# Kernel optimization log

Hardware: AMD Instinct MI355X
Metric: run time of the kernel (lower is better)

Reference implementation:

```python
import jax, jax.numpy as jnp
import numpy as np

B, S, HID = 4, 2048, 1024
H, DH = 16, 64  # HID = H * DH
ADP, NTASKS = 64, 10
GATE_S = 100.0  # s (soft gate temperature), != smax=400 so no hard threshold


def setup_inputs() -> dict:
    key = jax.random.key(0)
    ks = jax.random.split(key, 13)
    sc = 0.02
    return {
        "hidden_states": jax.random.normal(ks[0], (B, S, HID), jnp.float32),
        "Wq": jax.random.normal(ks[1], (HID, HID), jnp.float32) * sc,
        "bq": jax.random.normal(ks[2], (HID,), jnp.float32) * sc,
        "Wk": jax.random.normal(ks[3], (HID, HID), jnp.float32) * sc,
        "bk": jax.random.normal(ks[4], (HID,), jnp.float32) * sc,
        "Wv": jax.random.normal(ks[5], (HID, HID), jnp.float32) * sc,
        "bv": jax.random.normal(ks[6], (HID,), jnp.float32) * sc,
        "fc1_w": jax.random.normal(ks[7], (HID, ADP), jnp.float32) * sc,
        "fc1_b": jax.random.normal(ks[8], (ADP,), jnp.float32) * sc,
        "fc2_w": jax.random.normal(ks[9], (ADP, HID), jnp.float32) * sc,
        "fc2_b": jax.random.normal(ks[10], (HID,), jnp.float32) * sc,
        "efc1": jax.random.normal(ks[11], (NTASKS, ADP), jnp.float32),
        "efc2": jax.random.normal(ks[12], (NTASKS, HID), jnp.float32),
        "t": 3,
    }


def reference(hidden_states, Wq, bq, Wk, bk, Wv, bv,
              fc1_w, fc1_b, fc2_w, fc2_b, efc1, efc2, t):
    x = hidden_states
    # --- parallel adapter with task gates (add_residual=False) ---
    gfc1 = jax.nn.sigmoid(GATE_S * efc1[t])  # [ADP]
    gfc2 = jax.nn.sigmoid(GATE_S * efc2[t])  # [HID]
    h = jax.nn.relu(x @ fc1_w + fc1_b) * gfc1          # [B,S,ADP]
    adapter_out = jax.nn.relu(h @ fc2_w + fc2_b) * gfc2  # [B,S,HID]
    # --- multi-head self-attention (absolute positions, no mask, eval dropout) ---
    def split_heads(y):  # [B,S,HID] -> [B,H,S,DH]
        return y.reshape(B, S, H, DH).transpose(0, 2, 1, 3)
    q = split_heads(x @ Wq + bq)
    k = split_heads(x @ Wk + bk)
    v = split_heads(x @ Wv + bv)
    scores = jnp.einsum("bhqd,bhkd->bhqk", q, k) / np.sqrt(DH).astype(jnp.float32)
    probs = jax.nn.softmax(scores, axis=-1)
    ctx = jnp.einsum("bhqk,bhkd->bhqd", probs, v)
    ctx = ctx.transpose(0, 2, 1, 3).reshape(B, S, HID)
    return ctx + adapter_out
```

## Files before the change

kernel.cpp:

```cpp
#include <hip/hip_runtime.h>
#include <stdint.h>
#include <stddef.h>

typedef unsigned short u16;
typedef unsigned int u32;
typedef __bf16 bf16x8 __attribute__((ext_vector_type(8)));
typedef __bf16 bf16x4 __attribute__((ext_vector_type(4)));
typedef short s16x4 __attribute__((ext_vector_type(4)));
typedef float f32x4 __attribute__((ext_vector_type(4)));

#define BB  4
#define SS  2048
#define HIDD 1024
#define NH  16
#define DHD 64

#define GLD16(gaddr, laddr) \
  __builtin_amdgcn_global_load_lds( \
      (const __attribute__((address_space(1))) u32*)(gaddr), \
      (__attribute__((address_space(3))) u32*)(laddr), 16, 0, 0)

#define LDS_BARRIER() asm volatile("s_waitcnt lgkmcnt(0)\n\ts_barrier" ::: "memory")

#if __has_builtin(__builtin_amdgcn_exp2f)
  #define EXP2(x) __builtin_amdgcn_exp2f(x)
#else
  #define EXP2(x) __expf((x) * 0.6931471805599453f)
#endif

__device__ __forceinline__ u16 f2b(float f){
  union { float f; unsigned u; } c; c.f = f;
  unsigned r = c.u + 0x7fffu + ((c.u >> 16) & 1u);
  return (u16)(r >> 16);
}
__device__ __forceinline__ f32x4 mfma32(bf16x8 a, bf16x8 b, f32x4 c){
  return __builtin_amdgcn_mfma_f32_16x16x32_bf16(a, b, c, 0, 0, 0);
}
__device__ __forceinline__ f32x4 mfma16(s16x4 a, s16x4 b, f32x4 c){
  return __builtin_amdgcn_mfma_f32_16x16x16bf16_1k(a, b, c, 0, 0, 0);
}

__global__ __launch_bounds__(256)
void prep(const float* __restrict__ x, u16* __restrict__ xb,
          const float* __restrict__ Wq, const float* __restrict__ Wk,
          const float* __restrict__ Wv, const float* __restrict__ f1w,
          const float* __restrict__ f2w,
          u16* __restrict__ wqkv, u16* __restrict__ wtf1, u16* __restrict__ wtf2)
{
  __shared__ float tile[32][33];
  int blk = blockIdx.x;
  const int tid = threadIdx.x;
  if (blk < 8192) {
    int i = blk * 1024 + tid * 4;
    float4 v = *reinterpret_cast<const float4*>(&x[i]);
    ushort4 o;
    o.x = f2b(v.x); o.y = f2b(v.y); o.z = f2b(v.z); o.w = f2b(v.w);
    *reinterpret_cast<ushort4*>(&xb[i]) = o;
    return;
  }
  blk -= 8192;
  if (blk >= 3200) {
    u16* pad = wqkv + (size_t)3136 * 1024;
    uint4 z = make_uint4(0u, 0u, 0u, 0u);
    *reinterpret_cast<uint4*>(&pad[(size_t)(blk - 3200) * 2048 + tid * 8]) = z;
    return;
  }
  const float* in; u16* out; int R, C, c0, r0;
  if (blk < 3072) {
    int m = blk >> 10, t = blk & 1023;
    in = (m == 0) ? Wq : (m == 1) ? Wk : Wv;
    out = wqkv + (size_t)m * 1024 * 1024;
    R = 1024; C = 1024; c0 = (t & 31) * 32; r0 = (t >> 5) * 32;
  } else if (blk < 3136) {
    int t = blk - 3072;
    in = f1w; out = wtf1; R = 1024; C = 64;
    c0 = (t & 1) * 32; r0 = (t >> 1) * 32;
  } else {
    int t = blk - 3136;
    in = f2w; out = wtf2; R = 64; C = 1024;
    c0 = (t & 31) * 32; r0 = (t >> 5) * 32;
  }
  int tx = tid & 31, ty = tid >> 5;
  #pragma unroll
  for (int j = 0; j < 32; j += 8)
    tile[ty + j][tx] = in[(size_t)(r0 + ty + j) * C + c0 + tx];
  __syncthreads();
  #pragma unroll
  for (int j = 0; j < 32; j += 8)
    out[(size_t)(c0 + ty + j) * R + r0 + tx] = f2b(tile[tx][ty + j]);
}

__global__ __launch_bounds__(256)
void gemm_qkv(const u16* __restrict__ X, const u16* __restrict__ Wt,
              const float* __restrict__ bq, const float* __restrict__ bk,
              const float* __restrict__ bv,
              const float* __restrict__ f1b, const float* __restrict__ efc1,
              const int* __restrict__ tptr,
              u16* __restrict__ qb, u16* __restrict__ kb, u16* __restrict__ vt,
              u16* __restrict__ hb)
{
  constexpr int K = 1024;
  __shared__ __align__(16) u16 ldsX[128 * 32];
  __shared__ __align__(16) u16 ldsW[128 * 32];
  const int tid = threadIdx.x;
  const int w = tid >> 6, lane = tid & 63, quad = lane >> 4, ln = lane & 15;
  const int m0 = blockIdx.y * 128, n0 = blockIdx.x * 128;
  const int wrow = (w >> 1) * 64;
  const int wcol = (w & 1) * 64;
  const int srow = tid >> 2;
  const int scol = (tid & 3) * 8;

  f32x4 acc[4][4] = {};

  for (int k0 = 0; k0 < K; k0 += 32) {
    #pragma unroll
    for (int c = 0; c < 2; ++c)
      GLD16(&X[(size_t)(m0 + c * 64 + srow) * K + k0 + scol], &ldsX[c * 2048 + w * 512]);
    #pragma unroll
    for (int c = 0; c < 2; ++c)
      GLD16(&Wt[(size_t)(n0 + c * 64 + srow) * K + k0 + scol], &ldsW[c * 2048 + w * 512]);
    __syncthreads();

    bf16x8 a[4], bfr[4];
    #pragma unroll
    for (int mt = 0; mt < 4; ++mt)
      a[mt] = *reinterpret_cast<const bf16x8*>(&ldsX[(wrow + mt * 16 + ln) * 32 + quad * 8]);
    #pragma unroll
    for (int nt = 0; nt < 4; ++nt)
      bfr[nt] = *reinterpret_cast<const bf16x8*>(&ldsW[(wcol + nt * 16 + ln) * 32 + quad * 8]);
    #pragma unroll
    for (int mt = 0; mt < 4; ++mt)
      #pragma unroll
      for (int nt = 0; nt < 4; ++nt)
        acc[mt][nt] = mfma32(a[mt], bfr[nt], acc[mt][nt]);
    __syncthreads();
  }

  if (n0 < 2048) {
    const float scale = (n0 < 1024) ? 0.18033688f : 1.f;
    const float* bias = (n0 < 1024) ? bq : bk;
    u16* dst = (n0 < 1024) ? qb : kb;
    const int nb = n0 & 1023;
    #pragma unroll
    for (int nt = 0; nt < 4; ++nt) {
      const int col = nb + wcol + nt * 16 + ln;
      const float bvv = bias[col];
      #pragma unroll
      for (int mt = 0; mt < 4; ++mt)
        #pragma unroll
        for (int r = 0; r < 4; ++r) {
          int row = m0 + wrow + mt * 16 + quad * 4 + r;
          dst[(size_t)row * 1024 + col] = f2b((acc[mt][nt][r] + bvv) * scale);
        }
    }
  } else if (n0 < 3072) {
    #pragma unroll
    for (int nt = 0; nt < 4; ++nt) {
      const int colv = (n0 - 2048) + wcol + nt * 16 + ln;
      const float bvv = bv[colv];
      const int h = colv >> 6, d = colv & 63;
      #pragma unroll
      for (int mt = 0; mt < 4; ++mt) {
        int row = m0 + wrow + mt * 16 + quad * 4;
        int bb = row >> 11, s = row & 2047;
        ushort4 o;
        o.x = f2b(acc[mt][nt][0] + bvv);
        o.y = f2b(acc[mt][nt][1] + bvv);
        o.z = f2b(acc[mt][nt][2] + bvv);
        o.w = f2b(acc[mt][nt][3] + bvv);
        *reinterpret_cast<ushort4*>(
            &vt[((((size_t)bb * NH + h) * DHD + d) << 11) + s]) = o;
      }
    }
  } else if (wcol == 0) {
    int t = tptr[0];
    if ((unsigned)t > 9u) t = 0;
    #pragma unroll
    for (int nt = 0; nt < 4; ++nt) {
      const int col = nt * 16 + ln;
      const float bvv = f1b[col];
      const float g = 1.f / (1.f + __expf(-100.f * efc1[t * 64 + col]));
      #pragma unroll
      for (int mt = 0; mt < 4; ++mt)
        #pragma unroll
        for (int r = 0; r < 4; ++r) {
          int row = m0 + wrow + mt * 16 + quad * 4 + r;
          hb[(size_t)row * 64 + col] = f2b(fmaxf(acc[mt][nt][r] + bvv, 0.f) * g);
        }
    }
  }
}

__global__ __launch_bounds__(256, 4)
void attn(const u16* __restrict__ Q, const u16* __restrict__ Kb,
          const u16* __restrict__ Vt, const u16* __restrict__ hb,
          const u16* __restrict__ w2, const float* __restrict__ b2,
          const float* __restrict__ gate2, const int* __restrict__ tptr,
          float* __restrict__ out)
{
  __shared__ __align__(16) u16 ldsK[64 * 72];
  __shared__ __align__(16) u16 ldsV[64 * 76];

  const int tid = threadIdx.x;
  const int w = tid >> 6, lane = tid & 63, quad = lane >> 4, ln = lane & 15;
  const int h = blockIdx.x, b = blockIdx.y, qt = blockIdx.z;
  const int bh = b * NH + h;
  const int qbase = qt * 128 + w * 32;
  const int skey = tid >> 3;
  const int sd   = (tid & 7) * 8;

  bf16x8 qf[2][2];
  #pragma unroll
  for (int q2 = 0; q2 < 2; ++q2)
    #pragma unroll
    for (int kk = 0; kk < 2; ++kk)
      qf[q2][kk] = *reinterpret_cast<const bf16x8*>(
          &Q[(size_t)(b * SS + qbase + q2 * 16 + ln) * HIDD + h * DHD + kk * 32 + quad * 8]);

  f32x4 o[4][2] = {};
  f32x4 lacc[2] = {};
  const s16x4 ones = {0x3F80, 0x3F80, 0x3F80, 0x3F80};

  const u16* Kp = &Kb[(size_t)(b * SS + skey) * HIDD + h * DHD + sd];
  const u16* Vp = &Vt[((size_t)bh * DHD + skey) * SS + sd];

  uint4 rK0 = *reinterpret_cast<const uint4*>(Kp);
  uint4 rK1 = *reinterpret_cast<const uint4*>(Kp + (size_t)32 * HIDD);
  uint4 rV0 = *reinterpret_cast<const uint4*>(Vp);
  uint4 rV1 = *reinterpret_cast<const uint4*>(Vp + (size_t)32 * SS);

  for (int kt = 0; kt < SS; kt += 64) {
    LDS_BARRIER();
    *reinterpret_cast<uint4*>(&ldsK[skey * 72 + sd])        = rK0;
    *reinterpret_cast<uint4*>(&ldsK[(32 + skey) * 72 + sd]) = rK1;
    *reinterpret_cast<uint4*>(&ldsV[skey * 76 + sd])        = rV0;
    *reinterpret_cast<uint4*>(&ldsV[(32 + skey) * 76 + sd]) = rV1;
    if (kt + 64 < SS) {
      const u16* Kn = Kp + (size_t)(kt + 64) * HIDD;
      const u16* Vn = Vp + (kt + 64);
      rK0 = *reinterpret_cast<const uint4*>(Kn);
      rK1 = *reinterpret_cast<const uint4*>(Kn + (size_t)32 * HIDD);
      rV0 = *reinterpret_cast<const uint4*>(Vn);
      rV1 = *reinterpret_cast<const uint4*>(Vn + (size_t)32 * SS);
    }
    LDS_BARRIER();

    f32x4 s[4][2];
    __builtin_amdgcn_s_setprio(1);
    #pragma unroll
    for (int k4 = 0; k4 < 4; ++k4) {
      bf16x8 kf0 = *reinterpret_cast<const bf16x8*>(&ldsK[(k4 * 16 + ln) * 72 + quad * 8]);
      bf16x8 kf1 = *reinterpret_cast<const bf16x8*>(&ldsK[(k4 * 16 + ln) * 72 + 32 + quad * 8]);
      #pragma unroll
      for (int q2 = 0; q2 < 2; ++q2) {
        f32x4 z = {0.f, 0.f, 0.f, 0.f};
        z = mfma32(kf0, qf[q2][0], z);
        z = mfma32(kf1, qf[q2][1], z);
        s[k4][q2] = z;
      }
    }
    __builtin_amdgcn_s_setprio(0);

    s16x4 p[4][2];
    #pragma unroll
    for (int k4 = 0; k4 < 4; ++k4)
      #pragma unroll
      for (int q2 = 0; q2 < 2; ++q2) {
        union { bf16x4 b; s16x4 s; } cv;
        #pragma unroll
        for (int r = 0; r < 4; ++r)
          cv.b[r] = (__bf16)EXP2(s[k4][q2][r]);
        p[k4][q2] = cv.s;
      }

    __builtin_amdgcn_s_setprio(1);
    #pragma unroll
    for (int dt = 0; dt < 4; ++dt) {
      #pragma unroll
      for (int ks = 0; ks < 4; ++ks) {
        s16x4 vf = *reinterpret_cast<const s16x4*>(
            &ldsV[(dt * 16 + ln) * 76 + ks * 16 + quad * 4]);
        #pragma unroll
        for (int q2 = 0; q2 < 2; ++q2)
          o[dt][q2] = mfma16(vf, p[ks][q2], o[dt][q2]);
      }
    }
    #pragma unroll
    for (int ks = 0; ks < 4; ++ks)
      #pragma unroll
      for (int q2 = 0; q2 < 2; ++q2)
        lacc[q2] = mfma16(ones, p[ks][q2], lacc[q2]);
    __builtin_amdgcn_s_setprio(0);
  }

  float rl[2];
  #pragma unroll
  for (int q2 = 0; q2 < 2; ++q2)
    rl[q2] = 1.f / lacc[q2][0];

  f32x4 acc2[4][2] = {};
  #pragma unroll
  for (int kk = 0; kk < 2; ++kk) {
    bf16x8 hf[2];
    #pragma unroll
    for (int q2 = 0; q2 < 2; ++q2) {
      int q = qbase + q2 * 16 + ln;
      hf[q2] = *reinterpret_cast<const bf16x8*>(
          &hb[(size_t)(b * SS + q) * 64 + kk * 32 + quad * 8]);
    }
    #pragma unroll
    for (int dt = 0; dt < 4; ++dt) {
      bf16x8 wf = *reinterpret_cast<const bf16x8*>(
          &w2[(size_t)(h * DHD + dt * 16 + ln) * 64 + kk * 32 + quad * 8]);
      #pragma unroll
      for (int q2 = 0; q2 < 2; ++q2)
        acc2[dt][q2] = mfma32(wf, hf[q2], acc2[dt][q2]);
    }
  }

  int t = tptr[0];
  if ((unsigned)t > 9u) t = 0;
  float bv2[4][4], gv2[4][4];
  #pragma unroll
  for (int dt = 0; dt < 4; ++dt)
    #pragma unroll
    for (int r = 0; r < 4; ++r) {
      int col = h * DHD + dt * 16 + quad * 4 + r;
      bv2[dt][r] = b2[col];
      gv2[dt][r] = 1.f / (1.f + __expf(-100.f * gate2[t * HIDD + col]));
    }

  #pragma unroll
  for (int q2 = 0; q2 < 2; ++q2) {
    const int q = qbase + q2 * 16 + ln;
    float* orow = &out[(size_t)(b * SS + q) * HIDD + h * DHD];
    #pragma unroll
    for (int dt = 0; dt < 4; ++dt)
      #pragma unroll
      for (int r = 0; r < 4; ++r) {
        int d = dt * 16 + quad * 4 + r;
        float ad = fmaxf(acc2[dt][q2][r] + bv2[dt][r], 0.f) * gv2[dt][r];
        orow[d] = o[dt][q2][r] * rl[q2] + ad;
      }
  }
}

extern "C" void kernel_launch(void* const* d_in, const int* in_sizes, int n_in,
                              void* d_out, int out_size, void* d_ws, size_t ws_size,
                              hipStream_t stream) {
  const float* x    = (const float*)d_in[0];
  const float* Wq   = (const float*)d_in[1];
  const float* bq   = (const float*)d_in[2];
  const float* Wk   = (const float*)d_in[3];
  const float* bk   = (const float*)d_in[4];
  const float* Wv   = (const float*)d_in[5];
  const float* bv   = (const float*)d_in[6];
  const float* f1w  = (const float*)d_in[7];
  const float* f1b  = (const float*)d_in[8];
  const float* f2w  = (const float*)d_in[9];
  const float* f2b_ = (const float*)d_in[10];
  const float* efc1 = (const float*)d_in[11];
  const float* efc2 = (const float*)d_in[12];
  const int*   tptr = (const int*)d_in[13];
  float* out = (float*)d_out;

  unsigned char* ws = (unsigned char*)d_ws;
  u16* xb   = (u16*)(ws + 0);
  u16* wqkv = (u16*)(ws + (16u << 20));
  u16* wtf1 = wqkv + (size_t)3072 * 1024;
  u16* wtf2 = (u16*)(ws + (22u << 20) + (256u << 10));
  u16* hb   = (u16*)(ws + (23u << 20));
  u16* qb   = (u16*)(ws + (24u << 20));
  u16* kb   = (u16*)(ws + (40u << 20));
  u16* vt   = (u16*)(ws + (56u << 20));

  prep<<<dim3(11424), 256, 0, stream>>>(x, xb, Wq, Wk, Wv, f1w, f2w,
                                        wqkv, wtf1, wtf2);

  gemm_qkv<<<dim3(25, 64), 256, 0, stream>>>(xb, wqkv, bq, bk, bv,
                                             f1b, efc1, tptr, qb, kb, vt, hb);

  attn<<<dim3(NH, BB, SS / 128), 256, 0, stream>>>(
      qb, kb, vt, hb, wtf2, f2b_, efc2, tptr, out);
}
```

Measured before the change: 292.1 us.

## Double-buffer QKV GEMM, swizzle blocks, and compute softmax sums on VALU

The QKV GEMM now double-buffers its LDS tiles so the global-to-LDS loads for the next K slice are issued before computing the current one. It also uses a 1D grid with a swizzled block-to-tile mapping to improve L2 reuse. In attention, the row sums come from per-lane VALU accumulation of the fp32 exponentials plus a cross-lane shuffle, replacing extra MFMAs against a ones vector. The exp-to-bf16 conversion uses a cheaper rounding, and the s_setprio hints are removed. Doubled LDS may reduce GEMM occupancy, and the denominator now uses unrounded fp32 values while the numerator uses bf16-rounded ones.

```diff
diff --git a/kernel.cpp b/kernel.cpp
--- a/kernel.cpp
+++ b/kernel.cpp
@@ -5,7 +5,6 @@
 typedef unsigned short u16;
 typedef unsigned int u32;
 typedef __bf16 bf16x8 __attribute__((ext_vector_type(8)));
-typedef __bf16 bf16x4 __attribute__((ext_vector_type(4)));
 typedef short s16x4 __attribute__((ext_vector_type(4)));
 typedef float f32x4 __attribute__((ext_vector_type(4)));
 
@@ -32,6 +31,10 @@
   union { float f; unsigned u; } c; c.f = f;
   unsigned r = c.u + 0x7fffu + ((c.u >> 16) & 1u);
   return (u16)(r >> 16);
+}
+__device__ __forceinline__ u16 f2b_fast(float f){
+  union { float f; unsigned u; } c; c.f = f;
+  return (u16)((c.u + 0x8000u) >> 16);
 }
 __device__ __forceinline__ f32x4 mfma32(bf16x8 a, bf16x8 b, f32x4 c){
   return __builtin_amdgcn_mfma_f32_16x16x32_bf16(a, b, c, 0, 0, 0);
@@ -100,11 +103,14 @@
               u16* __restrict__ hb)
 {
   constexpr int K = 1024;
-  __shared__ __align__(16) u16 ldsX[128 * 32];
-  __shared__ __align__(16) u16 ldsW[128 * 32];
+  __shared__ __align__(16) u16 ldsX[2][128 * 32];
+  __shared__ __align__(16) u16 ldsW[2][128 * 32];
   const int tid = threadIdx.x;
   const int w = tid >> 6, lane = tid & 63, quad = lane >> 4, ln = lane & 15;
-  const int m0 = blockIdx.y * 128, n0 = blockIdx.x * 128;
+  const int id = blockIdx.x;
+  const int swz = (id & 7) * 200 + (id >> 3);
+  const int m0 = (swz / 25) * 128;
+  const int n0 = (swz % 25) * 128;
   const int wrow = (w >> 1) * 64;
   const int wcol = (w & 1) * 64;
   const int srow = tid >> 2;
@@ -112,27 +118,40 @@
 
   f32x4 acc[4][4] = {};
 
-  for (int k0 = 0; k0 < K; k0 += 32) {
-    #pragma unroll
-    for (int c = 0; c < 2; ++c)
-      GLD16(&X[(size_t)(m0 + c * 64 + srow) * K + k0 + scol], &ldsX[c * 2048 + w * 512]);
-    #pragma unroll
-    for (int c = 0; c < 2; ++c)
-      GLD16(&Wt[(size_t)(n0 + c * 64 + srow) * K + k0 + scol], &ldsW[c * 2048 + w * 512]);
-    __syncthreads();
+  #pragma unroll
+  for (int c = 0; c < 2; ++c) {
+    GLD16(&X[(size_t)(m0 + c * 64 + srow) * K + scol], &ldsX[0][c * 2048 + w * 512]);
+    GLD16(&Wt[(size_t)(n0 + c * 64 + srow) * K + scol], &ldsW[0][c * 2048 + w * 512]);
+  }
+  __syncthreads();
+
+  int cur = 0;
+  for (int k0 = 0; k0 < K; k0 += 32, cur ^= 1) {
+    if (k0 + 32 < K) {
+      #pragma unroll
+      for (int c = 0; c < 2; ++c) {
+        GLD16(&X[(size_t)(m0 + c * 64 + srow) * K + k0 + 32 + scol],
+              &ldsX[cur ^ 1][c * 2048 + w * 512]);
+        GLD16(&Wt[(size_t)(n0 + c * 64 + srow) * K + k0 + 32 + scol],
+              &ldsW[cur ^ 1][c * 2048 + w * 512]);
+      }
+    }
 
     bf16x8 a[4], bfr[4];
     #pragma unroll
     for (int mt = 0; mt < 4; ++mt)
-      a[mt] = *reinterpret_cast<const bf16x8*>(&ldsX[(wrow + mt * 16 + ln) * 32 + quad * 8]);
+      a[mt] = *reinterpret_cast<const bf16x8*>(
+          &ldsX[cur][(wrow + mt * 16 + ln) * 32 + quad * 8]);
     #pragma unroll
     for (int nt = 0; nt < 4; ++nt)
-      bfr[nt] = *reinterpret_cast<const bf16x8*>(&ldsW[(wcol + nt * 16 + ln) * 32 + quad * 8]);
+      bfr[nt] = *reinterpret_cast<const bf16x8*>(
+          &ldsW[cur][(wcol + nt * 16 + ln) * 32 + quad * 8]);
     #pragma unroll
     for (int mt = 0; mt < 4; ++mt)
       #pragma unroll
       for (int nt = 0; nt < 4; ++nt)
         acc[mt][nt] = mfma32(a[mt], bfr[nt], acc[mt][nt]);
+
     __syncthreads();
   }
 
@@ -218,8 +237,7 @@
           &Q[(size_t)(b * SS + qbase + q2 * 16 + ln) * HIDD + h * DHD + kk * 32 + quad * 8]);
 
   f32x4 o[4][2] = {};
-  f32x4 lacc[2] = {};
-  const s16x4 ones = {0x3F80, 0x3F80, 0x3F80, 0x3F80};
+  float lsum[2] = {0.f, 0.f};
 
   const u16* Kp = &Kb[(size_t)(b * SS + skey) * HIDD + h * DHD + sd];
   const u16* Vp = &Vt[((size_t)bh * DHD + skey) * SS + sd];
@@ -246,7 +264,6 @@
     LDS_BARRIER();
 
     f32x4 s[4][2];
-    __builtin_amdgcn_s_setprio(1);
     #pragma unroll
     for (int k4 = 0; k4 < 4; ++k4) {
       bf16x8 kf0 = *reinterpret_cast<const bf16x8*>(&ldsK[(k4 * 16 + ln) * 72 + quad * 8]);
@@ -259,21 +276,19 @@
         s[k4][q2] = z;
       }
     }
-    __builtin_amdgcn_s_setprio(0);
 
     s16x4 p[4][2];
     #pragma unroll
     for (int k4 = 0; k4 < 4; ++k4)
       #pragma unroll
-      for (int q2 = 0; q2 < 2; ++q2) {
-        union { bf16x4 b; s16x4 s; } cv;
+      for (int q2 = 0; q2 < 2; ++q2)
         #pragma unroll
-        for (int r = 0; r < 4; ++r)
-          cv.b[r] = (__bf16)EXP2(s[k4][q2][r]);
-        p[k4][q2] = cv.s;
-      }
-
-    __builtin_amdgcn_s_setprio(1);
+        for (int r = 0; r < 4; ++r) {
+          float pv = EXP2(s[k4][q2][r]);
+          lsum[q2] += pv;
+          p[k4][q2][r] = (short)f2b_fast(pv);
+        }
+
     #pragma unroll
     for (int dt = 0; dt < 4; ++dt) {
       #pragma unroll
@@ -285,18 +300,16 @@
           o[dt][q2] = mfma16(vf, p[ks][q2], o[dt][q2]);
       }
     }
-    #pragma unroll
-    for (int ks = 0; ks < 4; ++ks)
-      #pragma unroll
-      for (int q2 = 0; q2 < 2; ++q2)
-        lacc[q2] = mfma16(ones, p[ks][q2], lacc[q2]);
-    __builtin_amdgcn_s_setprio(0);
   }
 
   float rl[2];
   #pragma unroll
-  for (int q2 = 0; q2 < 2; ++q2)
-    rl[q2] = 1.f / lacc[q2][0];
+  for (int q2 = 0; q2 < 2; ++q2) {
+    float v = lsum[q2];
+    v += __shfl_xor(v, 16);
+    v += __shfl_xor(v, 32);
+    rl[q2] = 1.f / v;
+  }
 
   f32x4 acc2[4][2] = {};
   #pragma unroll
@@ -377,8 +390,8 @@
   prep<<<dim3(11424), 256, 0, stream>>>(x, xb, Wq, Wk, Wv, f1w, f2w,
                                         wqkv, wtf1, wtf2);
 
-  gemm_qkv<<<dim3(25, 64), 256, 0, stream>>>(xb, wqkv, bq, bk, bv,
-                                             f1b, efc1, tptr, qb, kb, vt, hb);
+  gemm_qkv<<<dim3(1600), 256, 0, stream>>>(xb, wqkv, bq, bk, bv,
+                                           f1b, efc1, tptr, qb, kb, vt, hb);
 
   attn<<<dim3(NH, BB, SS / 128), 256, 0, stream>>>(
       qb, kb, vt, hb, wtf2, f2b_, efc2, tptr, out);
```

New measurement: 292.9 us. About the same (+0.3%).
